# Kernel optimization log

Hardware: AMD Instinct MI355X
Metric: run time of the kernel (lower is better)

## Reference

```python
import jax, jax.numpy as jnp
import numpy as np

N, E, C, RB, H = 10000, 160000, 64, 8, 64
AVG_NEIGH = 16.0


def _sph(v):
    # component-normalized real spherical harmonics l=1,2,3 of unit vectors v [E,3]
    x, y, z = v[..., 0], v[..., 1], v[..., 2]
    s3, s5, s15 = 3.0 ** 0.5, 5.0 ** 0.5, 15.0 ** 0.5
    y1 = s3 * jnp.stack([x, y, z], -1)  # [E,3]
    y2 = jnp.stack([
        s15 * x * y,
        s15 * y * z,
        0.5 * s5 * (3.0 * z * z - 1.0),
        s15 * x * z,
        0.5 * s15 * (x * x - y * y),
    ], -1)  # [E,5]
    c1 = (35.0 / 8.0) ** 0.5
    c2 = 105.0 ** 0.5
    c3 = (21.0 / 8.0) ** 0.5
    c4 = (7.0 ** 0.5) / 2.0
    y3 = jnp.stack([
        c1 * y * (3.0 * x * x - y * y),
        c2 * x * y * z,
        c3 * y * (5.0 * z * z - 1.0),
        c4 * z * (5.0 * z * z - 3.0),
        c3 * x * (5.0 * z * z - 1.0),
        0.5 * c2 * z * (x * x - y * y),
        c1 * x * (x * x - y * y),
    ], -1)  # [E,7]
    return y1, y2, y3


def setup_inputs() -> dict:
    key = jax.random.key(0)
    ks = jax.random.split(key, 12)
    inp = {
        'vectors': jax.random.normal(ks[0], (E, 3), jnp.float32),
        'node_feats': jax.random.normal(ks[1], (N, C), jnp.float32),
        'radial_embedding': jax.random.normal(ks[2], (E, RB), jnp.float32),
        'W_up': jax.random.normal(ks[3], (C, C), jnp.float32) / np.sqrt(C),
        'mlp_w1': jax.random.normal(ks[4], (RB, H), jnp.float32) / np.sqrt(RB),
        'mlp_w2': jax.random.normal(ks[5], (H, H), jnp.float32) / np.sqrt(H),
        'mlp_w3': jax.random.normal(ks[6], (H, H), jnp.float32) / np.sqrt(H),
        'mlp_w4': jax.random.normal(ks[7], (H, 4 * C), jnp.float32) / np.sqrt(H),
        'W_down': jax.random.normal(ks[8], (4, C, C), jnp.float32) / np.sqrt(C),
        'senders': jax.random.randint(ks[9], (E,), 0, N, jnp.int32),
        'receivers': jax.random.randint(ks[10], (E,), 0, N, jnp.int32),
    }
    return inp


def reference(vectors, node_feats, radial_embedding, W_up, mlp_w1, mlp_w2, mlp_w3, mlp_w4, W_down, senders, receivers):
    n = node_feats.shape[0]
    # linear_up (scalars: plain channel mixing)
    x = node_feats @ W_up                                   # [N,C]
    sf = x[senders]                                         # [E,C] gather
    u = vectors / (jnp.linalg.norm(vectors, axis=-1, keepdims=True) + 1e-12)
    y1, y2, y3 = _sph(u)
    # radial MLP -> per-irrep mixing weights [E, 4C]
    h = jax.nn.silu(radial_embedding @ mlp_w1)
    h = jax.nn.silu(h @ mlp_w2)
    h = jax.nn.silu(h @ mlp_w3)
    mix = h @ mlp_w4
    m0, m1, m2, m3 = jnp.split(mix, 4, axis=-1)             # each [E,C]
    # tensor product of Cx0e with Y_l -> Cx(l), scaled by radial mix
    msg0 = sf * m0                                          # [E,C]
    msg1 = (sf * m1)[:, :, None] * y1[:, None, :]           # [E,C,3]
    msg2 = (sf * m2)[:, :, None] * y2[:, None, :]           # [E,C,5]
    msg3 = (sf * m3)[:, :, None] * y3[:, None, :]           # [E,C,7]
    inv = 1.0 / jnp.sqrt(jnp.asarray(AVG_NEIGH, msg0.dtype))
    seg = lambda m: jax.ops.segment_sum(m, receivers, num_segments=n) * inv
    o0, o1, o2, o3 = seg(msg0), seg(msg1), seg(msg2), seg(msg3)
    # linear_down: per-l channel mixing
    o0 = o0 @ W_down[0]
    o1 = jnp.einsum('ncm,cd->ndm', o1, W_down[1])
    o2 = jnp.einsum('ncm,cd->ndm', o2, W_down[2])
    o3 = jnp.einsum('ncm,cd->ndm', o3, W_down[3])
    return jnp.concatenate([o0, o1.reshape(n, -1), o2.reshape(n, -1), o3.reshape(n, -1)], axis=-1)  # [N, 16C]
```

## Files before the change

### kernel.cpp

```cpp
#include <hip/hip_runtime.h>
#include <math.h>

#define CC 64
typedef _Float16 f16;
typedef _Float16 half8_t __attribute__((ext_vector_type(8)));
typedef float f32x4 __attribute__((ext_vector_type(4)));

__device__ __forceinline__ float silu_f(float v) {
    return v / (1.0f + __expf(-v));
}

__global__ void k_up(const float* __restrict__ nf, const float* __restrict__ Wup,
                     float* __restrict__ x, int N) {
    int tid = blockIdx.x * blockDim.x + threadIdx.x;
    if (tid >= N * CC) return;
    int n = tid >> 6;
    int j = tid & 63;
    const float* nfr = nf + (size_t)n * CC;
    float acc = 0.f;
#pragma unroll
    for (int k = 0; k < CC; ++k) acc += nfr[k] * Wup[k * CC + j];
    x[tid] = acc;
}

__global__ void k_wt(const float* __restrict__ w1, const float* __restrict__ w2,
                     const float* __restrict__ w3, const float* __restrict__ w4,
                     f16* __restrict__ wT1, f16* __restrict__ wT2,
                     f16* __restrict__ wT3, f16* __restrict__ wT4) {
    int i = blockIdx.x * 256 + threadIdx.x;
    if (i < 2048) {
        int n = i >> 5, k = i & 31;
        wT1[i] = (k < 8) ? (f16)w1[k * 64 + n] : (f16)0.f;
    } else if (i < 6144) {
        int j = i - 2048; int n = j >> 6, k = j & 63;
        wT2[j] = (f16)w2[k * 64 + n];
    } else if (i < 10240) {
        int j = i - 6144; int n = j >> 6, k = j & 63;
        wT3[j] = (f16)w3[k * 64 + n];
    } else if (i < 26624) {
        int j = i - 10240; int l = j >> 12; int r = j & 4095;
        int n = r >> 6, k = r & 63;
        wT4[j] = (f16)w4[k * 256 + l * 64 + n];
    }
}

__global__ void k_hist(const int* __restrict__ rcv, int* __restrict__ cnt, int E) {
    int e = blockIdx.x * blockDim.x + threadIdx.x;
    if (e < E) atomicAdd(&cnt[rcv[e]], 1);
}

__global__ __launch_bounds__(1024) void k_scan(const int* __restrict__ cnt,
        int* __restrict__ off, int* __restrict__ cur, int N) {
    __shared__ int wsum[16];
    int t = threadIdx.x;
    int wave = t >> 6, lane = t & 63;
    int per = (N + 1023) >> 10;
    int i0 = t * per;
    int s = 0;
    for (int j = 0; j < per; ++j) {
        int i = i0 + j;
        if (i < N) s += cnt[i];
    }
    int sc = s;
#pragma unroll
    for (int d = 1; d < 64; d <<= 1) {
        int u = __shfl_up(sc, d, 64);
        if (lane >= d) sc += u;
    }
    if (lane == 63) wsum[wave] = sc;
    __syncthreads();
    if (wave == 0) {
        int v = (lane < 16) ? wsum[lane] : 0;
        int s2 = v;
#pragma unroll
        for (int d = 1; d < 16; d <<= 1) {
            int u = __shfl_up(s2, d, 64);
            if (lane >= d) s2 += u;
        }
        if (lane < 16) wsum[lane] = s2;
    }
    __syncthreads();
    int base = ((wave > 0) ? wsum[wave - 1] : 0) + (sc - s);
    int run = base;
    for (int j = 0; j < per; ++j) {
        int i = i0 + j;
        if (i < N) { off[i] = run; cur[i] = run; run += cnt[i]; }
    }
    if (t == 1023) off[N] = run;
}

__global__ void k_fill(const int* __restrict__ rcv, const int* __restrict__ snd,
                       const float* __restrict__ vec, int* __restrict__ cur,
                       int* __restrict__ eid, int* __restrict__ sndp,
                       float* __restrict__ yb, int E) {
    int e = blockIdx.x * blockDim.x + threadIdx.x;
    if (e >= E) return;
    int p = atomicAdd(&cur[rcv[e]], 1);
    eid[p] = e;
    sndp[p] = snd[e];

    float vx = vec[(size_t)e * 3 + 0];
    float vy = vec[(size_t)e * 3 + 1];
    float vz = vec[(size_t)e * 3 + 2];
    float nrm = sqrtf(vx * vx + vy * vy + vz * vz) + 1e-12f;
    float rinv = 1.0f / nrm;
    float ux = vx * rinv, uy = vy * rinv, uz = vz * rinv;

    const float s3 = 1.7320508075688772f;
    const float s5 = 2.2360679774997896f;
    const float s15 = 3.8729833462074170f;
    const float c1 = 2.0916500663351889f;
    const float c2 = 10.246950765959598f;
    const float c3 = 1.6201851746019651f;
    const float c4 = 1.3228756555322954f;

    float zz = uz * uz, xx = ux * ux, yy = uy * uy;
    float4 r0 = {1.0f, s3 * ux, s3 * uy, s3 * uz};
    float4 r1 = {s15 * ux * uy, s15 * uy * uz, 0.5f * s5 * (3.f * zz - 1.f),
                 s15 * ux * uz};
    float4 r2 = {0.5f * s15 * (xx - yy), c1 * uy * (3.f * xx - yy),
                 c2 * ux * uy * uz, c3 * uy * (5.f * zz - 1.f)};
    float4 r3 = {c4 * uz * (5.f * zz - 3.f), c3 * ux * (5.f * zz - 1.f),
                 0.5f * c2 * uz * (xx - yy), c1 * ux * (xx - yy)};
    float* yr = yb + (size_t)p * 16;
    *(float4*)(yr + 0)  = r0;
    *(float4*)(yr + 4)  = r1;
    *(float4*)(yr + 8)  = r2;
    *(float4*)(yr + 12) = r3;
}

__global__ __launch_bounds__(256) void k_mlp(const float* __restrict__ rad,
        const f16* __restrict__ wT1, const f16* __restrict__ wT2,
        const f16* __restrict__ wT3, const f16* __restrict__ wT4,
        const int* __restrict__ eid, f16* __restrict__ mixp, int E) {
    __shared__ f16 act[128][72];

    int t = threadIdx.x;
    int e0 = blockIdx.x * 128;
    int lane = t & 63;
    int wid = t >> 6;
    int m0 = wid * 32;
    int fm = lane & 15;
    int q  = lane >> 4;

    const half8_t hz = {0, 0, 0, 0, 0, 0, 0, 0};

    half8_t a0 = hz, a1 = hz;
    if (q == 0) {
        int ci0 = e0 + m0 + fm;
        if (ci0 < E) {
            int e = eid[ci0];
            float4 p0 = *(const float4*)(rad + (size_t)e * 8);
            float4 p1 = *(const float4*)(rad + (size_t)e * 8 + 4);
            a0 = (half8_t){(f16)p0.x, (f16)p0.y, (f16)p0.z, (f16)p0.w,
                           (f16)p1.x, (f16)p1.y, (f16)p1.z, (f16)p1.w};
        }
        int ci1 = e0 + m0 + 16 + fm;
        if (ci1 < E) {
            int e = eid[ci1];
            float4 p0 = *(const float4*)(rad + (size_t)e * 8);
            float4 p1 = *(const float4*)(rad + (size_t)e * 8 + 4);
            a1 = (half8_t){(f16)p0.x, (f16)p0.y, (f16)p0.z, (f16)p0.w,
                           (f16)p1.x, (f16)p1.y, (f16)p1.z, (f16)p1.w};
        }
    }
#pragma unroll
    for (int nt = 0; nt < 4; ++nt) {
        half8_t b = *(const half8_t*)(wT1 + ((nt * 16 + fm) << 5) + q * 8);
        f32x4 c0 = {0.f, 0.f, 0.f, 0.f};
        c0 = __builtin_amdgcn_mfma_f32_16x16x32_f16(a0, b, c0, 0, 0, 0);
        f32x4 c1 = {0.f, 0.f, 0.f, 0.f};
        c1 = __builtin_amdgcn_mfma_f32_16x16x32_f16(a1, b, c1, 0, 0, 0);
#pragma unroll
        for (int r = 0; r < 4; ++r) {
            act[m0 + q * 4 + r][nt * 16 + fm]      = (f16)silu_f(c0[r]);
            act[m0 + 16 + q * 4 + r][nt * 16 + fm] = (f16)silu_f(c1[r]);
        }
    }

    auto loadA = [&](int mbase, int kc) -> half8_t {
        return *(const half8_t*)&act[mbase + fm][kc + q * 8];
    };

    const f16* wts[2] = {wT2, wT3};
#pragma unroll
    for (int L = 0; L < 2; ++L) {
        const f16* wT = wts[L];
        half8_t a00 = loadA(m0, 0),      a01 = loadA(m0, 32);
        half8_t a10 = loadA(m0 + 16, 0), a11 = loadA(m0 + 16, 32);
#pragma unroll
        for (int nt = 0; nt < 4; ++nt) {
            const f16* wr = wT + ((nt * 16 + fm) << 6);
            half8_t b0 = *(const half8_t*)(wr + q * 8);
            half8_t b1 = *(const half8_t*)(wr + 32 + q * 8);
            f32x4 c0 = {0.f, 0.f, 0.f, 0.f};
            c0 = __builtin_amdgcn_mfma_f32_16x16x32_f16(a00, b0, c0, 0, 0, 0);
            c0 = __builtin_amdgcn_mfma_f32_16x16x32_f16(a01, b1, c0, 0, 0, 0);
            f32x4 c1 = {0.f, 0.f, 0.f, 0.f};
            c1 = __builtin_amdgcn_mfma_f32_16x16x32_f16(a10, b0, c1, 0, 0, 0);
            c1 = __builtin_amdgcn_mfma_f32_16x16x32_f16(a11, b1, c1, 0, 0, 0);
#pragma unroll
            for (int r = 0; r < 4; ++r) {
                act[m0 + q * 4 + r][nt * 16 + fm]      = (f16)silu_f(c0[r]);
                act[m0 + 16 + q * 4 + r][nt * 16 + fm] = (f16)silu_f(c1[r]);
            }
        }
    }

    half8_t A00 = loadA(m0, 0),      A01 = loadA(m0, 32);
    half8_t A10 = loadA(m0 + 16, 0), A11 = loadA(m0 + 16, 32);

#pragma unroll
    for (int l = 0; l < 4; ++l) {
        const f16* wT = wT4 + (l << 12);
#pragma unroll
        for (int nt = 0; nt < 4; ++nt) {
            const f16* wr = wT + ((nt * 16 + fm) << 6);
            half8_t b0 = *(const half8_t*)(wr + q * 8);
            half8_t b1 = *(const half8_t*)(wr + 32 + q * 8);
            f32x4 c0 = {0.f, 0.f, 0.f, 0.f};
            c0 = __builtin_amdgcn_mfma_f32_16x16x32_f16(A00, b0, c0, 0, 0, 0);
            c0 = __builtin_amdgcn_mfma_f32_16x16x32_f16(A01, b1, c0, 0, 0, 0);
            f32x4 c1 = {0.f, 0.f, 0.f, 0.f};
            c1 = __builtin_amdgcn_mfma_f32_16x16x32_f16(A10, b0, c1, 0, 0, 0);
            c1 = __builtin_amdgcn_mfma_f32_16x16x32_f16(A11, b1, c1, 0, 0, 0);
#pragma unroll
            for (int r = 0; r < 4; ++r) {
                act[m0 + q * 4 + r][nt * 16 + fm]      = (f16)c0[r];
                act[m0 + 16 + q * 4 + r][nt * 16 + fm] = (f16)c1[r];
            }
        }
#pragma unroll
        for (int it = 0; it < 4; ++it) {
            int row = (lane >> 3) + it * 8;
            int ci = e0 + m0 + row;
            if (ci < E) {
                half8_t v = *(const half8_t*)&act[m0 + row][(lane & 7) * 8];
                *(half8_t*)&mixp[(size_t)ci * 256 + l * 64 + (lane & 7) * 8] = v;
            }
        }
    }
}

__global__ __launch_bounds__(256) void k_gather(const float* __restrict__ x,
        const f16* __restrict__ mixp, const float* __restrict__ yb,
        const int* __restrict__ sndp, const int* __restrict__ off,
        const float* __restrict__ Wd, float* __restrict__ out, int N) {
    __shared__ float sbuf[4][64 * 20];
    int wv = threadIdx.x >> 6;
    int lane = threadIdx.x & 63;
    int n = blockIdx.x * 4 + wv;
    if (n >= N) return;

    float o[16];
#pragma unroll
    for (int i = 0; i < 16; ++i) o[i] = 0.f;

    auto process = [&](int i) {
        int s = sndp[i];
        const float* yr = yb + (size_t)i * 16;
        float4 A = *(const float4*)(yr + 0);
        float4 B = *(const float4*)(yr + 4);
        float4 Cv = *(const float4*)(yr + 8);
        float4 D = *(const float4*)(yr + 12);
        float sf = x[(size_t)s * 64 + lane];
        const f16* mr = mixp + (size_t)i * 256;
        float t0 = sf * (float)mr[lane];
        float t1 = sf * (float)mr[64 + lane];
        float t2 = sf * (float)mr[128 + lane];
        float t3 = sf * (float)mr[192 + lane];
        o[0]  += t0;
        o[1]  += t1 * A.y;
        o[2]  += t1 * A.z;
        o[3]  += t1 * A.w;
        o[4]  += t2 * B.x;
        o[5]  += t2 * B.y;
        o[6]  += t2 * B.z;
        o[7]  += t2 * B.w;
        o[8]  += t2 * Cv.x;
        o[9]  += t3 * Cv.y;
        o[10] += t3 * Cv.z;
        o[11] += t3 * Cv.w;
        o[12] += t3 * D.x;
        o[13] += t3 * D.y;
        o[14] += t3 * D.z;
        o[15] += t3 * D.w;
    };

    int beg = off[n], end = off[n + 1];
    int i = beg;
    for (; i + 1 < end; i += 2) { process(i); process(i + 1); }
    if (i < end) process(i);

    float* sw = sbuf[wv];
#pragma unroll
    for (int a = 0; a < 4; ++a) {
        f32x4 vq = {o[4 * a + 0], o[4 * a + 1], o[4 * a + 2], o[4 * a + 3]};
        *(f32x4*)&sw[lane * 20 + 4 * a] = vq;
    }

    f32x4 dA = {0.f, 0.f, 0.f, 0.f}, dB = dA, dC = dA, dD = dA;
#pragma unroll 1
    for (int c = 0; c < 64; ++c) {
        f32x4 q0 = *(const f32x4*)&sw[c * 20 + 0];
        f32x4 q1 = *(const f32x4*)&sw[c * 20 + 4];
        f32x4 q2 = *(const f32x4*)&sw[c * 20 + 8];
        f32x4 q3 = *(const f32x4*)&sw[c * 20 + 12];
        float w0  = Wd[c * 64 + lane];
        float w1r = Wd[4096 + c * 64 + lane];
        float w2r = Wd[8192 + c * 64 + lane];
        float w3r = Wd[12288 + c * 64 + lane];
        f32x4 wA = {w0, w1r, w1r, w1r};
        f32x4 wC4 = {w2r, w3r, w3r, w3r};
        dA += q0 * wA;
        dB += q1 * w2r;
        dC += q2 * wC4;
        dD += q3 * w3r;
    }

    float* outr = out + (size_t)n * 1024;
    outr[lane] = 0.25f * dA[0];
#pragma unroll
    for (int m = 0; m < 3; ++m) outr[64 + lane * 3 + m] = 0.25f * dA[1 + m];
    outr[256 + lane * 5 + 0] = 0.25f * dB[0];
    outr[256 + lane * 5 + 1] = 0.25f * dB[1];
    outr[256 + lane * 5 + 2] = 0.25f * dB[2];
    outr[256 + lane * 5 + 3] = 0.25f * dB[3];
    outr[256 + lane * 5 + 4] = 0.25f * dC[0];
    outr[576 + lane * 7 + 0] = 0.25f * dC[1];
    outr[576 + lane * 7 + 1] = 0.25f * dC[2];
    outr[576 + lane * 7 + 2] = 0.25f * dC[3];
    outr[576 + lane * 7 + 3] = 0.25f * dD[0];
    outr[576 + lane * 7 + 4] = 0.25f * dD[1];
    outr[576 + lane * 7 + 5] = 0.25f * dD[2];
    outr[576 + lane * 7 + 6] = 0.25f * dD[3];
}

extern "C" void kernel_launch(void* const* d_in, const int* in_sizes, int n_in,
                              void* d_out, int out_size, void* d_ws, size_t ws_size,
                              hipStream_t stream) {
    const float* vectors    = (const float*)d_in[0];
    const float* node_feats = (const float*)d_in[1];
    const float* radial     = (const float*)d_in[2];
    const float* W_up       = (const float*)d_in[3];
    const float* w1         = (const float*)d_in[4];
    const float* w2         = (const float*)d_in[5];
    const float* w3         = (const float*)d_in[6];
    const float* w4         = (const float*)d_in[7];
    const float* Wd         = (const float*)d_in[8];
    const int*   snd        = (const int*)d_in[9];
    const int*   rcv        = (const int*)d_in[10];
    float* out = (float*)d_out;

    int E = in_sizes[9];
    int N = in_sizes[1] / CC;

    f16*   wT1  = (f16*)d_ws;
    f16*   wT2  = wT1 + 2048;
    f16*   wT3  = wT2 + 4096;
    f16*   wT4  = wT3 + 4096;
    float* x    = (float*)(wT4 + 16384);
    float* yb   = x + (size_t)N * 64;
    f16*   mixp = (f16*)(yb + (size_t)E * 16);
    int*   cnt  = (int*)(mixp + (size_t)E * 256);
    int*   off  = cnt + N;
    int*   cur  = off + (N + 1);
    int*   eid  = cur + N;
    int*   sndp = eid + E;

    hipMemsetAsync(cnt, 0, (size_t)N * sizeof(int), stream);

    k_wt<<<(26624 + 255) / 256, 256, 0, stream>>>(w1, w2, w3, w4, wT1, wT2, wT3, wT4);
    k_up<<<(N * CC + 255) / 256, 256, 0, stream>>>(node_feats, W_up, x, N);
    k_hist<<<(E + 255) / 256, 256, 0, stream>>>(rcv, cnt, E);
    k_scan<<<1, 1024, 0, stream>>>(cnt, off, cur, N);
    k_fill<<<(E + 255) / 256, 256, 0, stream>>>(rcv, snd, vectors, cur, eid, sndp, yb, E);
    k_mlp<<<(E + 127) / 128, 256, 0, stream>>>(radial, wT1, wT2, wT3, wT4, eid, mixp, E);
    k_gather<<<(N + 3) / 4, 256, 0, stream>>>(x, mixp, yb, sndp, off, Wd, out, N);
}
```

Baseline: 251.5 us.

## Split each node's edge gather and down-projection across two wavefronts

The gather kernel now gives each node two wavefronts instead of one. Each wavefront accumulates half of the node's incoming edges, the two partial sums are combined in shared memory, and the down-projection's l components are split between the two waves. Sender indices are loaded once per 64-edge chunk and broadcast with shuffles instead of being re-read per edge. This doubles the parallelism per node and shortens the serial edge loop, at the cost of two block-wide barriers and twice as many blocks.

```diff
diff --git a/kernel.cpp b/kernel.cpp
--- a/kernel.cpp
+++ b/kernel.cpp
@@ -246,18 +246,26 @@
         const f16* __restrict__ mixp, const float* __restrict__ yb,
         const int* __restrict__ sndp, const int* __restrict__ off,
         const float* __restrict__ Wd, float* __restrict__ out, int N) {
-    __shared__ float sbuf[4][64 * 20];
-    int wv = threadIdx.x >> 6;
-    int lane = threadIdx.x & 63;
-    int n = blockIdx.x * 4 + wv;
-    if (n >= N) return;
+    __shared__ float sbuf[2][64 * 20];
+    int tid = threadIdx.x;
+    int lane = tid & 63;
+    int pr   = tid >> 7;
+    int h    = (tid >> 6) & 1;
+    int n = blockIdx.x * 2 + pr;
+    bool alive = (n < N);
 
     float o[16];
 #pragma unroll
     for (int i = 0; i < 16; ++i) o[i] = 0.f;
 
-    auto process = [&](int i) {
-        int s = sndp[i];
+    int beg = 0, end = 0;
+    if (alive) { beg = off[n]; end = off[n + 1]; }
+    int len = end - beg;
+    int half = (len + 1) >> 1;
+    int b0 = beg + (h ? half : 0);
+    int e1 = h ? end : (beg + half);
+
+    auto process = [&](int i, int s) {
         const float* yr = yb + (size_t)i * 16;
         float4 A = *(const float4*)(yr + 0);
         float4 B = *(const float4*)(yr + 4);
@@ -287,53 +295,83 @@
         o[15] += t3 * D.w;
     };
 
-    int beg = off[n], end = off[n + 1];
-    int i = beg;
-    for (; i + 1 < end; i += 2) { process(i); process(i + 1); }
-    if (i < end) process(i);
-
-    float* sw = sbuf[wv];
-#pragma unroll
-    for (int a = 0; a < 4; ++a) {
-        f32x4 vq = {o[4 * a + 0], o[4 * a + 1], o[4 * a + 2], o[4 * a + 3]};
-        *(f32x4*)&sw[lane * 20 + 4 * a] = vq;
-    }
-
-    f32x4 dA = {0.f, 0.f, 0.f, 0.f}, dB = dA, dC = dA, dD = dA;
+    for (int cb = b0; cb < e1; cb += 64) {
+        int m = e1 - cb; if (m > 64) m = 64;
+        int sv = (cb + lane < e1) ? sndp[cb + lane] : 0;
+        int j = 0;
+        for (; j + 1 < m; j += 2) {
+            int s0 = __shfl(sv, j, 64);
+            int s1 = __shfl(sv, j + 1, 64);
+            process(cb + j, s0);
+            process(cb + j + 1, s1);
+        }
+        if (j < m) process(cb + j, __shfl(sv, j, 64));
+    }
+
+    float* sw = sbuf[pr];
+    if (h == 0) {
+#pragma unroll
+        for (int a = 0; a < 4; ++a) {
+            f32x4 vq = {o[4 * a + 0], o[4 * a + 1], o[4 * a + 2], o[4 * a + 3]};
+            *(f32x4*)&sw[lane * 20 + 4 * a] = vq;
+        }
+    }
+    __syncthreads();
+    if (h == 1) {
+#pragma unroll
+        for (int a = 0; a < 4; ++a) {
+            f32x4 vq = *(const f32x4*)&sw[lane * 20 + 4 * a];
+            f32x4 ad = {o[4 * a + 0], o[4 * a + 1], o[4 * a + 2], o[4 * a + 3]};
+            vq += ad;
+            *(f32x4*)&sw[lane * 20 + 4 * a] = vq;
+        }
+    }
+    __syncthreads();
+
+    if (!alive) return;
+    float* outr = out + (size_t)n * 1024;
+
+    if (h == 0) {
+        f32x4 dA = {0.f, 0.f, 0.f, 0.f}, dB = dA;
 #pragma unroll 1
-    for (int c = 0; c < 64; ++c) {
-        f32x4 q0 = *(const f32x4*)&sw[c * 20 + 0];
-        f32x4 q1 = *(const f32x4*)&sw[c * 20 + 4];
-        f32x4 q2 = *(const f32x4*)&sw[c * 20 + 8];
-        f32x4 q3 = *(const f32x4*)&sw[c * 20 + 12];
-        float w0  = Wd[c * 64 + lane];
-        float w1r = Wd[4096 + c * 64 + lane];
-        float w2r = Wd[8192 + c * 64 + lane];
-        float w3r = Wd[12288 + c * 64 + lane];
-        f32x4 wA = {w0, w1r, w1r, w1r};
-        f32x4 wC4 = {w2r, w3r, w3r, w3r};
-        dA += q0 * wA;
-        dB += q1 * w2r;
-        dC += q2 * wC4;
-        dD += q3 * w3r;
-    }
-
-    float* outr = out + (size_t)n * 1024;
-    outr[lane] = 0.25f * dA[0];
-#pragma unroll
-    for (int m = 0; m < 3; ++m) outr[64 + lane * 3 + m] = 0.25f * dA[1 + m];
-    outr[256 + lane * 5 + 0] = 0.25f * dB[0];
-    outr[256 + lane * 5 + 1] = 0.25f * dB[1];
-    outr[256 + lane * 5 + 2] = 0.25f * dB[2];
-    outr[256 + lane * 5 + 3] = 0.25f * dB[3];
-    outr[256 + lane * 5 + 4] = 0.25f * dC[0];
-    outr[576 + lane * 7 + 0] = 0.25f * dC[1];
-    outr[576 + lane * 7 + 1] = 0.25f * dC[2];
-    outr[576 + lane * 7 + 2] = 0.25f * dC[3];
-    outr[576 + lane * 7 + 3] = 0.25f * dD[0];
-    outr[576 + lane * 7 + 4] = 0.25f * dD[1];
-    outr[576 + lane * 7 + 5] = 0.25f * dD[2];
-    outr[576 + lane * 7 + 6] = 0.25f * dD[3];
+        for (int c = 0; c < 64; ++c) {
+            f32x4 q0 = *(const f32x4*)&sw[c * 20 + 0];
+            f32x4 q1 = *(const f32x4*)&sw[c * 20 + 4];
+            float w0  = Wd[c * 64 + lane];
+            float w1r = Wd[4096 + c * 64 + lane];
+            float w2r = Wd[8192 + c * 64 + lane];
+            f32x4 wA = {w0, w1r, w1r, w1r};
+            dA += q0 * wA;
+            dB += q1 * w2r;
+        }
+        outr[lane] = 0.25f * dA[0];
+#pragma unroll
+        for (int m2 = 0; m2 < 3; ++m2) outr[64 + lane * 3 + m2] = 0.25f * dA[1 + m2];
+        outr[256 + lane * 5 + 0] = 0.25f * dB[0];
+        outr[256 + lane * 5 + 1] = 0.25f * dB[1];
+        outr[256 + lane * 5 + 2] = 0.25f * dB[2];
+        outr[256 + lane * 5 + 3] = 0.25f * dB[3];
+    } else {
+        f32x4 dC = {0.f, 0.f, 0.f, 0.f}, dD = dC;
+#pragma unroll 1
+        for (int c = 0; c < 64; ++c) {
+            f32x4 q2 = *(const f32x4*)&sw[c * 20 + 8];
+            f32x4 q3 = *(const f32x4*)&sw[c * 20 + 12];
+            float w2r = Wd[8192 + c * 64 + lane];
+            float w3r = Wd[12288 + c * 64 + lane];
+            f32x4 wC4 = {w2r, w3r, w3r, w3r};
+            dC += q2 * wC4;
+            dD += q3 * w3r;
+        }
+        outr[256 + lane * 5 + 4] = 0.25f * dC[0];
+        outr[576 + lane * 7 + 0] = 0.25f * dC[1];
+        outr[576 + lane * 7 + 1] = 0.25f * dC[2];
+        outr[576 + lane * 7 + 2] = 0.25f * dC[3];
+        outr[576 + lane * 7 + 3] = 0.25f * dD[0];
+        outr[576 + lane * 7 + 4] = 0.25f * dD[1];
+        outr[576 + lane * 7 + 5] = 0.25f * dD[2];
+        outr[576 + lane * 7 + 6] = 0.25f * dD[3];
+    }
 }
 
 extern "C" void kernel_launch(void* const* d_in, const int* in_sizes, int n_in,
@@ -376,5 +414,5 @@
     k_scan<<<1, 1024, 0, stream>>>(cnt, off, cur, N);
     k_fill<<<(E + 255) / 256, 256, 0, stream>>>(rcv, snd, vectors, cur, eid, sndp, yb, E);
     k_mlp<<<(E + 127) / 128, 256, 0, stream>>>(radial, wT1, wT2, wT3, wT4, eid, mixp, E);
-    k_gather<<<(N + 3) / 4, 256, 0, stream>>>(x, mixp, yb, sndp, off, Wd, out, N);
-}
+    k_gather<<<(N + 1) / 2, 256, 0, stream>>>(x, mixp, yb, sndp, off, Wd, out, N);
+}
```

New measurement: 281.3 us. 11.8% more time.
